# Kernel tuning notes

Measured on AMD Instinct MI355X. Metric: run time of the kernel, lower is better.

Reference implementation:

```python
import jax, jax.numpy as jnp
import numpy as np

B, T, D = 2, 2048, 1024
H, HD = 16, 64
MAX_LEN = 2048


def setup_inputs() -> dict:
    key = jax.random.key(0)
    ks = jax.random.split(key, 7)
    s = 0.02
    return {
        "x": jax.random.normal(ks[0], (B, T, D), dtype=jnp.float32),
        "qkv_w": jax.random.normal(ks[1], (3 * D, D), dtype=jnp.float32) * s,
        "qkv_b": jax.random.normal(ks[2], (3 * D,), dtype=jnp.float32) * s,
        "out_w": jax.random.normal(ks[3], (D, D), dtype=jnp.float32) * s,
        "out_b": jax.random.normal(ks[4], (D,), dtype=jnp.float32) * s,
        "rel_pos": jax.random.normal(ks[5], (2 * MAX_LEN - 1, HD), dtype=jnp.float32),
        "rpe_w": jax.random.normal(ks[6], (HD,), dtype=jnp.float32) * s,
    }


def reference(x, qkv_w, qkv_b, out_w, out_b, rel_pos, rpe_w):
    Bq, Tq, Dq = x.shape
    scale = HD ** -0.5
    qkv = x @ qkv_w.T + qkv_b  # [B,T,3D]
    qkv = qkv.reshape(Bq, Tq, 3, H, HD)
    q = qkv[:, :, 0].transpose(0, 2, 1, 3)  # [B,H,T,HD]
    k = qkv[:, :, 1].transpose(0, 2, 1, 3)
    v = qkv[:, :, 2].transpose(0, 2, 1, 3)
    scores = jnp.einsum('bhqd,bhkd->bhqk', q, k) * scale  # [B,H,T,T]
    # relative position bias: gather rel embeddings, project to scalar
    rel_idx = jnp.arange(Tq)[None, :] - jnp.arange(Tq)[:, None] + MAX_LEN - 1  # [T,T]
    bias = (rel_pos @ rpe_w)[rel_idx]  # project first (cheap), then gather -> [T,T]
    scores = scores + bias[None, None]
    attn = jax.nn.softmax(scores, axis=-1)
    out = jnp.einsum('bhqk,bhkd->bhqd', attn, v)  # [B,H,T,HD]
    out = out.transpose(0, 2, 1, 3).reshape(Bq, Tq, Dq)
    return out @ out_w.T + out_b
```

## Files before the change

### kernel.cpp

```cpp
#include <hip/hip_runtime.h>
#include <math.h>

#define B_ 2
#define T_ 2048
#define D_ 1024
#define H_ 16
#define HD_ 64
#define MAXLEN_ 2048
#define N3D_ 3072
#define M_ (B_ * T_)
#define KA 1024

#define SCALE_L2E 0.18033688011116215f
#define L2E 1.4426950408889634f

typedef unsigned short ushort_t;
typedef __attribute__((ext_vector_type(8))) short short8;
typedef __attribute__((ext_vector_type(4))) float floatx4;
#define MFMA16(a, b, c) __builtin_amdgcn_mfma_f32_16x16x32_bf16(a, b, c, 0, 0, 0)

static __device__ __forceinline__ ushort_t f2bf(float f) {
    unsigned u = __float_as_uint(f);
    unsigned r = (u + 0x7FFFu + ((u >> 16) & 1u)) >> 16;
    return (ushort_t)r;
}
static __device__ __forceinline__ unsigned packrnu(float a, float b) {
    unsigned ua = __float_as_uint(a) + 0x8000u;
    unsigned ub = __float_as_uint(b) + 0x8000u;
    return __builtin_amdgcn_perm(ub, ua, 0x07060302u);
}

static __device__ __forceinline__ void gld16(const ushort_t* g, ushort_t* l) {
    __builtin_amdgcn_global_load_lds(
        (const __attribute__((address_space(1))) void*)g,
        (__attribute__((address_space(3))) void*)l, 16, 0, 0);
}

__global__ __launch_bounds__(256) void cvt_all(
    const float* __restrict__ x, const float* __restrict__ qw,
    const float* __restrict__ ow, const float* __restrict__ rel_pos,
    const float* __restrict__ rpe_w,
    ushort_t* __restrict__ Xc, ushort_t* __restrict__ QWc,
    ushort_t* __restrict__ OWc, float* __restrict__ biasp)
{
    const int row = blockIdx.x;
    if (row < M_ + N3D_ + D_) {
        const float* src; ushort_t* dst; int r;
        if (row < M_)            { src = x;  dst = Xc;  r = row; }
        else if (row < M_ + N3D_){ src = qw; dst = QWc; r = row - M_; }
        else                     { src = ow; dst = OWc; r = row - M_ - N3D_; }
        const int c = threadIdx.x * 4;
        float4 v = *(const float4*)(src + (size_t)r * 1024 + c);
        ushort4 hv;
        hv.x = f2bf(v.x); hv.y = f2bf(v.y); hv.z = f2bf(v.z); hv.w = f2bf(v.w);
        *(ushort4*)(dst + (size_t)r * KA + c) = hv;
    } else {
        const int wv = threadIdx.x >> 6, lane = threadIdx.x & 63;
        const int r = (row - (M_ + N3D_ + D_)) * 4 + wv;
        if (r < 2 * MAXLEN_ - 1) {
            float v = rel_pos[(size_t)r * HD_ + lane] * rpe_w[lane];
#pragma unroll
            for (int off = 32; off; off >>= 1) v += __shfl_down(v, off);
            if (lane == 0) biasp[r] = v * L2E;
        }
    }
}

__global__ __launch_bounds__(256) void qkv_mfma(
    const ushort_t* __restrict__ Ac, const ushort_t* __restrict__ Bc,
    const float* __restrict__ bias,
    ushort_t* __restrict__ Qs, ushort_t* __restrict__ Khi,
    ushort_t* __restrict__ Vt)
{
    __shared__ __align__(16) ushort_t As[16 * 512];
    __shared__ __align__(16) ushort_t Bs[16 * 512];
    const int tid = threadIdx.x;
    const int wv = tid >> 6, lane = tid & 63;
    const int l16 = lane & 15, quad = lane >> 4;
    const int wm = wv & 1, wn = wv >> 1;
    const int m0 = blockIdx.y * 128, n0 = blockIdx.x * 128;

    floatx4 acc[4][4];
#pragma unroll
    for (int i = 0; i < 4; ++i)
#pragma unroll
        for (int j = 0; j < 4; ++j) acc[i][j] = (floatx4){0.f, 0.f, 0.f, 0.f};

    for (int k0 = 0; k0 < KA; k0 += 64) {
        __syncthreads();
#pragma unroll
        for (int c = 0; c < 4; ++c) {
            const int b = wv * 4 + c;
            const int i = b >> 1, ks = b & 1;
            const int k = k0 + ks * 32 + quad * 8;
            gld16(Ac + (size_t)(m0 + i * 16 + l16) * KA + k, As + b * 512);
            gld16(Bc + (size_t)(n0 + i * 16 + l16) * KA + k, Bs + b * 512);
        }
        __syncthreads();
#pragma unroll
        for (int ks = 0; ks < 2; ++ks) {
            short8 af[4], bf[4];
#pragma unroll
            for (int ii = 0; ii < 4; ++ii)
                af[ii] = *(const short8*)(As + ((wm * 4 + ii) * 2 + ks) * 512 + lane * 8);
#pragma unroll
            for (int jj = 0; jj < 4; ++jj)
                bf[jj] = *(const short8*)(Bs + ((wn * 4 + jj) * 2 + ks) * 512 + lane * 8);
#pragma unroll
            for (int ii = 0; ii < 4; ++ii)
#pragma unroll
                for (int jj = 0; jj < 4; ++jj)
                    acc[ii][jj] = MFMA16(af[ii], bf[jj], acc[ii][jj]);
        }
    }

#pragma unroll
    for (int ii = 0; ii < 4; ++ii) {
#pragma unroll
        for (int r = 0; r < 4; ++r) {
            const int m = m0 + wm * 64 + ii * 16 + quad * 4 + r;
            const int bb = m >> 11, t = m & 2047;
#pragma unroll
            for (int jj = 0; jj < 4; ++jj) {
                const int n = n0 + wn * 64 + jj * 16 + l16;
                const int c = n >> 10, h = (n >> 6) & 15, hd = n & 63;
                const float v = acc[ii][jj][r] + bias[n];
                const size_t idx = (((size_t)bb * H_ + h) * T_ + t) * HD_ + hd;
                if (c == 0) { Qs[idx] = f2bf(v * SCALE_L2E); }
                else if (c == 1) { Khi[idx] = f2bf(v); }
                else { Vt[(((size_t)bb * H_ + h) * HD_ + hd) * T_ + t] = f2bf(v); }
            }
        }
    }
}

__global__ __launch_bounds__(256) void out_mfma(
    const ushort_t* __restrict__ Ac, const ushort_t* __restrict__ Bc,
    const float* __restrict__ bias, float* __restrict__ Out)
{
    __shared__ __align__(16) ushort_t As[16 * 512];
    __shared__ __align__(16) ushort_t Bs[8 * 512];
    const int tid = threadIdx.x;
    const int wv = tid >> 6, lane = tid & 63;
    const int l16 = lane & 15, quad = lane >> 4;
    const int wm = wv & 1, wn = wv >> 1;
    const int m0 = blockIdx.y * 128, n0 = blockIdx.x * 64;

    floatx4 acc[4][2];
#pragma unroll
    for (int i = 0; i < 4; ++i)
#pragma unroll
        for (int j = 0; j < 2; ++j) acc[i][j] = (floatx4){0.f, 0.f, 0.f, 0.f};

    for (int k0 = 0; k0 < KA; k0 += 64) {
        __syncthreads();
#pragma unroll
        for (int c = 0; c < 4; ++c) {
            const int b = wv * 4 + c;
            const int i = b >> 1, ks = b & 1;
            const int k = k0 + ks * 32 + quad * 8;
            gld16(Ac + (size_t)(m0 + i * 16 + l16) * KA + k, As + b * 512);
        }
#pragma unroll
        for (int c = 0; c < 2; ++c) {
            const int b = wv * 2 + c;
            const int j = b >> 1, ks = b & 1;
            const int k = k0 + ks * 32 + quad * 8;
            gld16(Bc + (size_t)(n0 + j * 16 + l16) * KA + k, Bs + b * 512);
        }
        __syncthreads();
#pragma unroll
        for (int ks = 0; ks < 2; ++ks) {
            short8 af[4], bf[2];
#pragma unroll
            for (int ii = 0; ii < 4; ++ii)
                af[ii] = *(const short8*)(As + ((wm * 4 + ii) * 2 + ks) * 512 + lane * 8);
#pragma unroll
            for (int jj = 0; jj < 2; ++jj)
                bf[jj] = *(const short8*)(Bs + ((wn * 2 + jj) * 2 + ks) * 512 + lane * 8);
#pragma unroll
            for (int ii = 0; ii < 4; ++ii)
#pragma unroll
                for (int jj = 0; jj < 2; ++jj)
                    acc[ii][jj] = MFMA16(af[ii], bf[jj], acc[ii][jj]);
        }
    }

#pragma unroll
    for (int ii = 0; ii < 4; ++ii) {
#pragma unroll
        for (int r = 0; r < 4; ++r) {
            const int m = m0 + wm * 64 + ii * 16 + quad * 4 + r;
#pragma unroll
            for (int jj = 0; jj < 2; ++jj) {
                const int n = n0 + wn * 32 + jj * 16 + l16;
                Out[(size_t)m * D_ + n] = acc[ii][jj][r] + bias[n];
            }
        }
    }
}

__global__ __launch_bounds__(256) void attn_mfma(
    const ushort_t* __restrict__ Qs, const ushort_t* __restrict__ Khi,
    const ushort_t* __restrict__ Vt, const float* __restrict__ biasp,
    ushort_t* __restrict__ AOc)
{
    __shared__ __align__(16) ushort_t KS[2][8 * 512];
    __shared__ __align__(16) ushort_t VS[2][8 * 512];
    __shared__ __align__(16) ushort_t PS[4][2][1024];

    const int i = blockIdx.x;
    const int j = i >> 3;
    const int bh = (i & 7) + 8 * (j >> 4);
    const int q0 = (j & 15) * 128;
    const int tid = threadIdx.x;
    const int wv = tid >> 6, lane = tid & 63;
    const int l16 = lane & 15, quad = lane >> 4;

    const int qw = q0 + wv * 32;

    short8 qh[2][2];
#pragma unroll
    for (int u = 0; u < 2; ++u) {
        const size_t qoff = ((size_t)bh * T_ + qw + u * 16 + l16) * HD_ + quad * 8;
        qh[u][0] = *(const short8*)(Qs + qoff);
        qh[u][1] = *(const short8*)(Qs + qoff + 32);
    }

    float l_r[2] = {0.f, 0.f};
    floatx4 o_acc[4][2];
#pragma unroll
    for (int g2 = 0; g2 < 4; ++g2)
#pragma unroll
        for (int u = 0; u < 2; ++u) o_acc[g2][u] = (floatx4){0.f, 0.f, 0.f, 0.f};

    const ushort_t* gK = Khi + (size_t)bh * T_ * HD_;
    const ushort_t* gV = Vt + (size_t)bh * HD_ * T_;
    const int c0base = 2047 + quad * 4 - (qw + 16 + l16);
    const int qdbase = quad >> 1;

    const size_t kstage = (size_t)(wv * 16 + l16) * HD_ + quad * 8;
    const size_t vstage = (size_t)(wv * 16 + l16) * T_ + quad * 8;

    gld16(gK + kstage,      KS[0] + (wv * 2 + 0) * 512);
    gld16(gK + kstage + 32, KS[0] + (wv * 2 + 1) * 512);
    gld16(gV + vstage,      VS[0] + (wv * 2 + 0) * 512);
    gld16(gV + vstage + 32, VS[0] + (wv * 2 + 1) * 512);
    __syncthreads();

    for (int t = 0; t < 32; ++t) {
        const int k0 = t * 64;
        const int buf = t & 1, nbuf = buf ^ 1;

        float4 f4[5];
        {
            const float* bp = biasp + (c0base + k0);
#pragma unroll
            for (int z = 0; z < 5; ++z)
                __builtin_memcpy(&f4[z], bp + z * 16, 16);
        }

        if (t < 31) {
            const size_t koff = kstage + (size_t)(k0 + 64) * HD_;
            gld16(gK + koff,      KS[nbuf] + (wv * 2 + 0) * 512);
            gld16(gK + koff + 32, KS[nbuf] + (wv * 2 + 1) * 512);
            const size_t voff = vstage + (size_t)(k0 + 64);
            gld16(gV + voff,      VS[nbuf] + (wv * 2 + 0) * 512);
            gld16(gV + voff + 32, VS[nbuf] + (wv * 2 + 1) * 512);
        }

#pragma unroll
        for (int g = 0; g < 4; ++g) {
            const short8 kh0 = *(const short8*)(KS[buf] + (g * 2 + 0) * 512 + lane * 8);
            const short8 kh1 = *(const short8*)(KS[buf] + (g * 2 + 1) * 512 + lane * 8);
            const int qd = 2 * (g & 1) + qdbase;
#pragma unroll
            for (int u = 0; u < 2; ++u) {
                const float4 bbv = f4[g + 1 - u];
                floatx4 a = (floatx4){bbv.x, bbv.y, bbv.z, bbv.w};
                a = MFMA16(kh0, qh[u][0], a);
                a = MFMA16(kh1, qh[u][1], a);
                const float p0 = __builtin_amdgcn_exp2f(a[0]);
                const float p1 = __builtin_amdgcn_exp2f(a[1]);
                const float p2 = __builtin_amdgcn_exp2f(a[2]);
                const float p3 = __builtin_amdgcn_exp2f(a[3]);
                l_r[u] += (p0 + p1) + (p2 + p3);
                uint2 pkd;
                pkd.x = packrnu(p0, p1);
                pkd.y = packrnu(p2, p3);
                *(uint2*)(PS[wv][u] + (g >> 1) * 512 + (qd * 16 + l16) * 8 + (quad & 1) * 4) = pkd;
            }
        }

        short8 pf[2][2];
#pragma unroll
        for (int u = 0; u < 2; ++u) {
            pf[u][0] = *(const short8*)(PS[wv][u] + lane * 8);
            pf[u][1] = *(const short8*)(PS[wv][u] + 512 + lane * 8);
        }

#pragma unroll
        for (int g2 = 0; g2 < 4; ++g2) {
            const short8 v0 = *(const short8*)(VS[buf] + (g2 * 2 + 0) * 512 + lane * 8);
            const short8 v1 = *(const short8*)(VS[buf] + (g2 * 2 + 1) * 512 + lane * 8);
#pragma unroll
            for (int u = 0; u < 2; ++u) {
                o_acc[g2][u] = MFMA16(v0, pf[u][0], o_acc[g2][u]);
                o_acc[g2][u] = MFMA16(v1, pf[u][1], o_acc[g2][u]);
            }
        }
        __syncthreads();
    }

    const int bb2 = bh >> 4, h2 = bh & 15;
#pragma unroll
    for (int u = 0; u < 2; ++u) {
        l_r[u] += __shfl_xor(l_r[u], 16);
        l_r[u] += __shfl_xor(l_r[u], 32);
        const float inv = 1.0f / l_r[u];
        const size_t m = (size_t)bb2 * T_ + qw + u * 16 + l16;
#pragma unroll
        for (int g2 = 0; g2 < 4; ++g2) {
            uint2 pk;
            pk.x = packrnu(o_acc[g2][u][0] * inv, o_acc[g2][u][1] * inv);
            pk.y = packrnu(o_acc[g2][u][2] * inv, o_acc[g2][u][3] * inv);
            *(uint2*)(AOc + m * KA + h2 * 64 + g2 * 16 + quad * 4) = pk;
        }
    }
}

extern "C" void kernel_launch(void* const* d_in, const int* in_sizes, int n_in,
                              void* d_out, int out_size, void* d_ws, size_t ws_size,
                              hipStream_t stream)
{
    const float* x       = (const float*)d_in[0];
    const float* qkv_w   = (const float*)d_in[1];
    const float* qkv_b   = (const float*)d_in[2];
    const float* out_w   = (const float*)d_in[3];
    const float* out_b   = (const float*)d_in[4];
    const float* rel_pos = (const float*)d_in[5];
    const float* rpe_w   = (const float*)d_in[6];
    float* out = (float*)d_out;

    const size_t QE = (size_t)B_ * H_ * T_ * HD_;
    ushort_t* Qs  = (ushort_t*)d_ws;
    ushort_t* Khi = Qs  + QE;
    ushort_t* Vt  = Khi + QE;
    ushort_t* Xc  = Vt  + QE;
    ushort_t* QWc = Xc  + (size_t)M_ * KA;
    ushort_t* OWc = QWc + (size_t)N3D_ * KA;
    ushort_t* AOc = OWc + (size_t)D_ * KA;
    float* biasp  = (float*)(AOc + (size_t)M_ * KA);

    cvt_all<<<M_ + N3D_ + D_ + 1024, 256, 0, stream>>>(
        x, qkv_w, out_w, rel_pos, rpe_w, Xc, QWc, OWc, biasp);

    qkv_mfma<<<dim3(N3D_ / 128, M_ / 128), 256, 0, stream>>>(
        Xc, QWc, qkv_b, Qs, Khi, Vt);
    attn_mfma<<<512, 256, 0, stream>>>(Qs, Khi, Vt, biasp, AOc);
    out_mfma<<<dim3(D_ / 64, M_ / 128), 256, 0, stream>>>(
        AOc, OWc, out_b, out);
}
```

Baseline: 259.7 us.

## Double-buffer LDS tiles and swizzle block order in QKV and output GEMMs

```diff
diff --git a/kernel.cpp b/kernel.cpp
--- a/kernel.cpp
+++ b/kernel.cpp
@@ -72,13 +72,16 @@
     ushort_t* __restrict__ Qs, ushort_t* __restrict__ Khi,
     ushort_t* __restrict__ Vt)
 {
-    __shared__ __align__(16) ushort_t As[16 * 512];
-    __shared__ __align__(16) ushort_t Bs[16 * 512];
+    __shared__ __align__(16) ushort_t As[2][16 * 512];
+    __shared__ __align__(16) ushort_t Bs[2][16 * 512];
     const int tid = threadIdx.x;
     const int wv = tid >> 6, lane = tid & 63;
     const int l16 = lane & 15, quad = lane >> 4;
     const int wm = wv & 1, wn = wv >> 1;
-    const int m0 = blockIdx.y * 128, n0 = blockIdx.x * 128;
+
+    const int orig = blockIdx.y * 24 + blockIdx.x;
+    const int swz = (orig & 7) * 96 + (orig >> 3);
+    const int m0 = (swz / 24) * 128, n0 = (swz % 24) * 128;
 
     floatx4 acc[4][4];
 #pragma unroll
@@ -86,32 +89,40 @@
 #pragma unroll
         for (int j = 0; j < 4; ++j) acc[i][j] = (floatx4){0.f, 0.f, 0.f, 0.f};
 
-    for (int k0 = 0; k0 < KA; k0 += 64) {
-        __syncthreads();
+    auto stage = [&](int bufi, int kk) {
 #pragma unroll
         for (int c = 0; c < 4; ++c) {
             const int b = wv * 4 + c;
             const int i = b >> 1, ks = b & 1;
-            const int k = k0 + ks * 32 + quad * 8;
-            gld16(Ac + (size_t)(m0 + i * 16 + l16) * KA + k, As + b * 512);
-            gld16(Bc + (size_t)(n0 + i * 16 + l16) * KA + k, Bs + b * 512);
-        }
-        __syncthreads();
+            const int k = kk + ks * 32 + quad * 8;
+            gld16(Ac + (size_t)(m0 + i * 16 + l16) * KA + k, As[bufi] + b * 512);
+            gld16(Bc + (size_t)(n0 + i * 16 + l16) * KA + k, Bs[bufi] + b * 512);
+        }
+    };
+
+    stage(0, 0);
+    __syncthreads();
+
+#pragma unroll 1
+    for (int t = 0; t < 16; ++t) {
+        const int cur = t & 1;
+        if (t < 15) stage(cur ^ 1, (t + 1) * 64);
 #pragma unroll
         for (int ks = 0; ks < 2; ++ks) {
             short8 af[4], bf[4];
 #pragma unroll
             for (int ii = 0; ii < 4; ++ii)
-                af[ii] = *(const short8*)(As + ((wm * 4 + ii) * 2 + ks) * 512 + lane * 8);
+                af[ii] = *(const short8*)(As[cur] + ((wm * 4 + ii) * 2 + ks) * 512 + lane * 8);
 #pragma unroll
             for (int jj = 0; jj < 4; ++jj)
-                bf[jj] = *(const short8*)(Bs + ((wn * 4 + jj) * 2 + ks) * 512 + lane * 8);
+                bf[jj] = *(const short8*)(Bs[cur] + ((wn * 4 + jj) * 2 + ks) * 512 + lane * 8);
 #pragma unroll
             for (int ii = 0; ii < 4; ++ii)
 #pragma unroll
                 for (int jj = 0; jj < 4; ++jj)
                     acc[ii][jj] = MFMA16(af[ii], bf[jj], acc[ii][jj]);
         }
+        if (t < 15) __syncthreads();
     }
 
 #pragma unroll
@@ -138,13 +149,16 @@
     const ushort_t* __restrict__ Ac, const ushort_t* __restrict__ Bc,
     const float* __restrict__ bias, float* __restrict__ Out)
 {
-    __shared__ __align__(16) ushort_t As[16 * 512];
-    __shared__ __align__(16) ushort_t Bs[8 * 512];
+    __shared__ __align__(16) ushort_t As[2][16 * 512];
+    __shared__ __align__(16) ushort_t Bs[2][8 * 512];
     const int tid = threadIdx.x;
     const int wv = tid >> 6, lane = tid & 63;
     const int l16 = lane & 15, quad = lane >> 4;
     const int wm = wv & 1, wn = wv >> 1;
-    const int m0 = blockIdx.y * 128, n0 = blockIdx.x * 64;
+
+    const int orig = blockIdx.y * 16 + blockIdx.x;
+    const int swz = (orig & 7) * 64 + (orig >> 3);
+    const int m0 = (swz >> 4) * 128, n0 = (swz & 15) * 64;
 
     floatx4 acc[4][2];
 #pragma unroll
@@ -152,38 +166,46 @@
 #pragma unroll
         for (int j = 0; j < 2; ++j) acc[i][j] = (floatx4){0.f, 0.f, 0.f, 0.f};
 
-    for (int k0 = 0; k0 < KA; k0 += 64) {
-        __syncthreads();
+    auto stage = [&](int bufi, int kk) {
 #pragma unroll
         for (int c = 0; c < 4; ++c) {
             const int b = wv * 4 + c;
             const int i = b >> 1, ks = b & 1;
-            const int k = k0 + ks * 32 + quad * 8;
-            gld16(Ac + (size_t)(m0 + i * 16 + l16) * KA + k, As + b * 512);
+            const int k = kk + ks * 32 + quad * 8;
+            gld16(Ac + (size_t)(m0 + i * 16 + l16) * KA + k, As[bufi] + b * 512);
         }
 #pragma unroll
         for (int c = 0; c < 2; ++c) {
             const int b = wv * 2 + c;
             const int j = b >> 1, ks = b & 1;
-            const int k = k0 + ks * 32 + quad * 8;
-            gld16(Bc + (size_t)(n0 + j * 16 + l16) * KA + k, Bs + b * 512);
-        }
-        __syncthreads();
+            const int k = kk + ks * 32 + quad * 8;
+            gld16(Bc + (size_t)(n0 + j * 16 + l16) * KA + k, Bs[bufi] + b * 512);
+        }
+    };
+
+    stage(0, 0);
+    __syncthreads();
+
+#pragma unroll 1
+    for (int t = 0; t < 16; ++t) {
+        const int cur = t & 1;
+        if (t < 15) stage(cur ^ 1, (t + 1) * 64);
 #pragma unroll
         for (int ks = 0; ks < 2; ++ks) {
             short8 af[4], bf[2];
 #pragma unroll
             for (int ii = 0; ii < 4; ++ii)
-                af[ii] = *(const short8*)(As + ((wm * 4 + ii) * 2 + ks) * 512 + lane * 8);
+                af[ii] = *(const short8*)(As[cur] + ((wm * 4 + ii) * 2 + ks) * 512 + lane * 8);
 #pragma unroll
             for (int jj = 0; jj < 2; ++jj)
-                bf[jj] = *(const short8*)(Bs + ((wn * 2 + jj) * 2 + ks) * 512 + lane * 8);
+                bf[jj] = *(const short8*)(Bs[cur] + ((wn * 2 + jj) * 2 + ks) * 512 + lane * 8);
 #pragma unroll
             for (int ii = 0; ii < 4; ++ii)
 #pragma unroll
                 for (int jj = 0; jj < 2; ++jj)
                     acc[ii][jj] = MFMA16(af[ii], bf[jj], acc[ii][jj]);
         }
+        if (t < 15) __syncthreads();
     }
 
 #pragma unroll
```

New measurement: 257.9 us. Within noise of the previous version (-0.7%).
